# Optimization experiments

Measured on AMD Instinct MI355X. Metric: run time of the kernel, lower is better.

Reference implementation:

```python
import jax, jax.numpy as jnp
import numpy as np

V, H, L = 32000, 2048, 4
B, S = 4, 1024


def setup_inputs() -> dict:
    key = jax.random.key(0)
    ks = jax.random.split(key, 10)
    input_ids = jax.random.randint(ks[0], (B, S), 0, V)
    emb = jax.random.normal(ks[1], (V, H), dtype=jnp.float32)
    # ternary quantized weights in {-1, 0, +1}, stored as int8
    layer_wq = jax.random.randint(ks[2], (L, H, H), -1, 2).astype(jnp.int8)
    layer_scale = jax.random.normal(ks[3], (L, H, 1), dtype=jnp.float32)
    layer_bias = jax.random.normal(ks[4], (L, H), dtype=jnp.float32)
    out_wq = jax.random.randint(ks[5], (V, H), -1, 2).astype(jnp.int8)
    out_scale = jax.random.normal(ks[6], (V, 1), dtype=jnp.float32)
    out_bias = jax.random.normal(ks[7], (V,), dtype=jnp.float32)
    return {
        "input_ids": input_ids,
        "emb": emb,
        "layer_wq": layer_wq,
        "layer_scale": layer_scale,
        "layer_bias": layer_bias,
        "out_wq": out_wq,
        "out_scale": out_scale,
        "out_bias": out_bias,
    }


def _bit_linear(x, wq, scale, bias):
    # dequantize ternary int8 weight: [out,in] * [out,1] -> fp32, then x @ W^T + b
    w = wq.astype(jnp.float32) * scale
    return jnp.einsum("bsh,oh->bso", x, w) + bias


def reference(input_ids, emb, layer_wq, layer_scale, layer_bias, out_wq, out_scale, out_bias):
    x = emb[input_ids]  # [B,S,H]
    for i in range(L):
        x = jax.nn.relu(_bit_linear(x, layer_wq[i], layer_scale[i], layer_bias[i]))
    logits = _bit_linear(x, out_wq, out_scale, out_bias)  # [B,S,V]
    return logits
```

## Files before the change

kernel.cpp:

```cpp
#include <hip/hip_runtime.h>
#include <hip/hip_bf16.h>
#include <stdint.h>
#include <stddef.h>

#define GLOBAL_AS __attribute__((address_space(1)))
#define LDS_AS __attribute__((address_space(3)))

typedef __attribute__((ext_vector_type(4))) float f32x4;
typedef __attribute__((ext_vector_type(8))) short bf16x8;
typedef __attribute__((ext_vector_type(4))) int   i32x4;

template<int N> struct ICn { static constexpr int value = N; };

__device__ __forceinline__ unsigned short f2bf(float f) {
  unsigned u = __float_as_uint(f);
  u += 0x7FFFu + ((u >> 16) & 1u);
  return (unsigned short)(u >> 16);
}

__device__ __forceinline__ void load_lds16(const void* g, void* l) {
  __builtin_amdgcn_global_load_lds((const GLOBAL_AS void*)g, (LDS_AS void*)l, 16, 0, 0);
}

template<int IMM, typename T>
__device__ __forceinline__ void ds_read128t(T &d, unsigned addr) {
  asm volatile("ds_read_b128 %0, %1 offset:%c2"
               : "=&v"(d) : "v"(addr), "i"(IMM));
}

#define SBAR0 __builtin_amdgcn_sched_barrier(0)

#define WAITV(N) do { SBAR0; \
  asm volatile("s_waitcnt vmcnt(" #N ")" ::: "memory"); SBAR0; } while (0)

#define WAITVL(N) do { SBAR0; \
  asm volatile("s_waitcnt vmcnt(" #N ") lgkmcnt(0)" ::: "memory"); SBAR0; } while (0)

#define LGKMW(N) do { SBAR0; \
  asm volatile("s_waitcnt lgkmcnt(" #N ")" ::: "memory"); SBAR0; } while (0)

__global__ __launch_bounds__(256) void detect_dtype_k(const int* __restrict__ w,
                                                      int* __restrict__ flag) {
  __shared__ int bad;
  if (threadIdx.x == 0) bad = 0;
  __syncthreads();
  int b = 0;
  for (int i = threadIdx.x; i < 4096; i += 256) {
    int v = w[i];
    if (v < -1 || v > 1) b = 1;
  }
  if (b) bad = 1;
  __syncthreads();
  if (threadIdx.x == 0) *flag = bad ? 0 : 1;
}

__global__ __launch_bounds__(256) void gather_emb_k(const int* __restrict__ ids,
                                                    const float* __restrict__ emb,
                                                    unsigned short* __restrict__ x) {
  const int t = blockIdx.x;
  const int row = ids[t];
  const float4* src = (const float4*)(emb + (size_t)row * 2048);
  const int e = threadIdx.x;
  float4 a = src[e * 2], b = src[e * 2 + 1];
  uint4 o;
  o.x = f2bf(a.x) | ((unsigned)f2bf(a.y) << 16);
  o.y = f2bf(a.z) | ((unsigned)f2bf(a.w) << 16);
  o.z = f2bf(b.x) | ((unsigned)f2bf(b.y) << 16);
  o.w = f2bf(b.z) | ((unsigned)f2bf(b.w) << 16);
  *(uint4*)(x + (size_t)t * 2048 + e * 8) = o;
}

__global__ __launch_bounds__(256) void convert_w_k(const void* __restrict__ src,
                                                   unsigned short* __restrict__ dst,
                                                   const int* __restrict__ flag) {
  const long long idx = ((long long)blockIdx.x * 256 + threadIdx.x) * 8;
  int v[8];
  if (*flag) {
    const int* s = (const int*)src + idx;
    const int4 a = *(const int4*)s;
    const int4 b = *(const int4*)(s + 4);
    v[0] = a.x; v[1] = a.y; v[2] = a.z; v[3] = a.w;
    v[4] = b.x; v[5] = b.y; v[6] = b.z; v[7] = b.w;
  } else {
    const uint2 u = *(const uint2*)((const char*)src + idx);
    v[0] = (char)(u.x); v[1] = (char)(u.x >> 8); v[2] = (char)(u.x >> 16); v[3] = (char)(u.x >> 24);
    v[4] = (char)(u.y); v[5] = (char)(u.y >> 8); v[6] = (char)(u.y >> 16); v[7] = (char)(u.y >> 24);
  }
  unsigned short o[8];
  #pragma unroll
  for (int k = 0; k < 8; ++k)
    o[k] = (v[k] == 0) ? 0 : ((v[k] > 0) ? 0x3F80 : 0xBF80);
  uint4 w;
  w.x = o[0] | ((unsigned)o[1] << 16);
  w.y = o[2] | ((unsigned)o[3] << 16);
  w.z = o[4] | ((unsigned)o[5] << 16);
  w.w = o[6] | ((unsigned)o[7] << 16);
  *(uint4*)(dst + idx) = w;
}

__global__ __launch_bounds__(256) void pack_w8_k(const void* __restrict__ src,
                                                 signed char* __restrict__ dst,
                                                 const int* __restrict__ flag) {
  if (!*flag) return;
  const long long idx = ((long long)blockIdx.x * 256 + threadIdx.x) * 8;
  const int* s = (const int*)src + idx;
  const int4 a = *(const int4*)s;
  const int4 b = *(const int4*)(s + 4);
  uint2 o;
  o.x = ((unsigned)(unsigned char)(signed char)a.x)       |
        ((unsigned)(unsigned char)(signed char)a.y << 8)  |
        ((unsigned)(unsigned char)(signed char)a.z << 16) |
        ((unsigned)(unsigned char)(signed char)a.w << 24);
  o.y = ((unsigned)(unsigned char)(signed char)b.x)       |
        ((unsigned)(unsigned char)(signed char)b.y << 8)  |
        ((unsigned)(unsigned char)(signed char)b.z << 16) |
        ((unsigned)(unsigned char)(signed char)b.w << 24);
  *(uint2*)(dst + idx) = o;
}

__global__ __launch_bounds__(256) void colsum_k(const signed char* __restrict__ wp,
                                                const signed char* __restrict__ wr,
                                                const int* __restrict__ flag,
                                                float* __restrict__ cs) {
  const signed char* w = (*flag) ? wp : wr;
  const int lane = threadIdx.x & 63;
  const int c = blockIdx.x * 4 + (threadIdx.x >> 6);
  const int4* p = (const int4*)(w + (size_t)c * 2048 + lane * 32);
  const int4 a = p[0], b = p[1];
  int wds[8] = {a.x, a.y, a.z, a.w, b.x, b.y, b.z, b.w};
  int s = 0;
  #pragma unroll
  for (int k = 0; k < 8; ++k)
    #pragma unroll
    for (int bb = 0; bb < 4; ++bb)
      s += (signed char)(wds[k] >> (8 * bb));
  #pragma unroll
  for (int o = 32; o; o >>= 1) s += __shfl_xor(s, o);
  if (lane == 0) cs[c] = (float)s;
}

__global__ __launch_bounds__(256) void rowquant_k(const unsigned short* __restrict__ x,
                                                  signed char* __restrict__ xq,
                                                  float* __restrict__ srow) {
  __shared__ float wmax[4];
  const int r = blockIdx.x;
  const int e = threadIdx.x;
  const uint4 u = *(const uint4*)(x + (size_t)r * 2048 + e * 8);
  unsigned wds[4] = {u.x, u.y, u.z, u.w};
  float v[8];
  #pragma unroll
  for (int k = 0; k < 4; ++k) {
    v[2 * k]     = __uint_as_float(wds[k] << 16);
    v[2 * k + 1] = __uint_as_float(wds[k] & 0xFFFF0000u);
  }
  float m = 0.0f;
  #pragma unroll
  for (int k = 0; k < 8; ++k) m = fmaxf(m, v[k]);
  #pragma unroll
  for (int o = 32; o; o >>= 1) m = fmaxf(m, __shfl_xor(m, o));
  if ((threadIdx.x & 63) == 0) wmax[threadIdx.x >> 6] = m;
  __syncthreads();
  const float mx = fmaxf(fmaxf(wmax[0], wmax[1]), fmaxf(wmax[2], wmax[3]));
  const float inv = mx > 0.0f ? 255.0f / mx : 0.0f;
  unsigned b[8];
  #pragma unroll
  for (int k = 0; k < 8; ++k) {
    int q = __float2int_rn(v[k] * inv - 127.5f);
    q = q < -128 ? -128 : (q > 127 ? 127 : q);
    b[k] = (unsigned)(unsigned char)(signed char)q;
  }
  uint2 o;
  o.x = b[0] | (b[1] << 8) | (b[2] << 16) | (b[3] << 24);
  o.y = b[4] | (b[5] << 8) | (b[6] << 16) | (b[7] << 24);
  *(uint2*)(xq + (size_t)r * 2048 + e * 8) = o;
  if (threadIdx.x == 0) srow[r] = mx * (1.0f / 255.0f);
}

__global__ __launch_bounds__(256, 2) void gemm_bt2_k(
    const unsigned short* __restrict__ A,
    const unsigned short* __restrict__ Bw,
    const float* __restrict__ scale,
    const float* __restrict__ bias,
    unsigned short* __restrict__ Cout,
    int M, int N, int K)
{
  __shared__ unsigned short As[2 * 8192];
  __shared__ unsigned short Bs[2 * 8192];

  const int tid  = threadIdx.x;
  const int lane = tid & 63;
  const int wid  = tid >> 6;
  const int wm   = wid >> 1;
  const int wn   = wid & 1;
  const int l15  = lane & 15;
  const int l4   = lane >> 4;

  const int mBase = blockIdx.y * 128;
  const int nBase = blockIdx.x * 128;

  const int gsw = ((lane & 7) ^ (lane >> 3)) * 8;

  const unsigned asB = (unsigned)(size_t)(const LDS_AS unsigned short*)As;
  const unsigned bsB = (unsigned)(size_t)(const LDS_AS unsigned short*)Bs;
  const unsigned x7  = (unsigned)(l15 & 7);
  const unsigned vA0 = asB + (wm << 13) + l15 * 128 + ((((unsigned)l4    ) ^ x7) << 4);
  const unsigned vA1 = asB + (wm << 13) + l15 * 128 + ((((unsigned)l4 + 4) ^ x7) << 4);
  const unsigned vB0 = bsB + (wn << 13) + l15 * 128 + ((((unsigned)l4    ) ^ x7) << 4);
  const unsigned vB1 = bsB + (wn << 13) + l15 * 128 + ((((unsigned)l4 + 4) ^ x7) << 4);

  const unsigned short* pA[4];
  const unsigned short* pB[4];
  #pragma unroll
  for (int j = 0; j < 4; ++j) {
    const int row = (wid * 4 + j) * 8 + (lane >> 3);
    pA[j] = A  + (size_t)(mBase + row) * K + gsw;
    pB[j] = Bw + (size_t)(nBase + row) * K + gsw;
  }

  f32x4 acc[4][4];
  #pragma unroll
  for (int i = 0; i < 4; ++i)
    #pragma unroll
    for (int j = 0; j < 4; ++j)
      acc[i][j] = (f32x4){0.f, 0.f, 0.f, 0.f};

  const int nt = K >> 6;

  #pragma unroll
  for (int j = 0; j < 4; ++j)
    load_lds16(pA[j], As + (wid * 4 + j) * 512);
  #pragma unroll
  for (int j = 0; j < 4; ++j)
    load_lds16(pB[j], Bs + (wid * 4 + j) * 512);
  #pragma unroll
  for (int j = 0; j < 4; ++j) { pA[j] += 64; pB[j] += 64; }
  WAITV(0);
  __builtin_amdgcn_s_barrier();

  bf16x8 afA[4], afB[4], bfrA[4], bfrB[4];

  for (int t = 0; t < nt; ++t) {
    const unsigned po = (unsigned)(t & 1) * 16384u;
    const unsigned aA0 = vA0 + po, aA1 = vA1 + po;
    const unsigned aB0 = vB0 + po, aB1 = vB1 + po;
    unsigned short* dA = As + (size_t)((t + 1) & 1) * 8192;
    unsigned short* dB = Bs + (size_t)((t + 1) & 1) * 8192;
    const bool st = (t + 1 < nt);

    ds_read128t<0   >(afA[0], aA0); ds_read128t<2048>(afA[1], aA0);
    ds_read128t<4096>(afA[2], aA0); ds_read128t<6144>(afA[3], aA0);
    ds_read128t<0   >(bfrA[0], aB0); ds_read128t<2048>(bfrA[1], aB0);
    ds_read128t<4096>(bfrA[2], aB0); ds_read128t<6144>(bfrA[3], aB0);
    ds_read128t<0   >(afB[0], aA1); ds_read128t<2048>(afB[1], aA1);
    ds_read128t<4096>(afB[2], aA1); ds_read128t<6144>(afB[3], aA1);
    ds_read128t<0   >(bfrB[0], aB1); ds_read128t<2048>(bfrB[1], aB1);
    ds_read128t<4096>(bfrB[2], aB1); ds_read128t<6144>(bfrB[3], aB1);
    #pragma unroll
    for (int j = 0; j < 4; ++j)
      load_lds16(st ? pA[j] : A, dA + (wid * 4 + j) * 512);
    #pragma unroll
    for (int j = 0; j < 4; ++j)
      load_lds16(st ? pB[j] : Bw, dB + (wid * 4 + j) * 512);
    #pragma unroll
    for (int j = 0; j < 4; ++j) { pA[j] += 64; pB[j] += 64; }

    LGKMW(8);
    __builtin_amdgcn_s_setprio(1);
    #pragma unroll
    for (int i = 0; i < 4; ++i)
      #pragma unroll
      for (int j = 0; j < 4; ++j)
        acc[i][j] = __builtin_amdgcn_mfma_f32_16x16x32_bf16(afA[i], bfrA[j], acc[i][j], 0, 0, 0);
    __builtin_amdgcn_s_setprio(0);
    SBAR0;
    LGKMW(0);
    __builtin_amdgcn_s_setprio(1);
    #pragma unroll
    for (int i = 0; i < 4; ++i)
      #pragma unroll
      for (int j = 0; j < 4; ++j)
        acc[i][j] = __builtin_amdgcn_mfma_f32_16x16x32_bf16(afB[i], bfrB[j], acc[i][j], 0, 0, 0);
    __builtin_amdgcn_s_setprio(0);
    SBAR0;
    WAITV(0);
    __builtin_amdgcn_s_barrier();
  }

  const int lr = l4;
  const int lc = l15;
  #pragma unroll
  for (int j = 0; j < 4; ++j) {
    const int col = nBase + wn * 64 + j * 16 + lc;
    const float sc = scale[col];
    const float bs = bias[col];
    #pragma unroll
    for (int i = 0; i < 4; ++i) {
      const int r0 = mBase + wm * 64 + i * 16 + lr * 4;
      #pragma unroll
      for (int r = 0; r < 4; ++r) {
        float vv = fmaxf(acc[i][j][r] * sc + bs, 0.0f);
        Cout[(size_t)(r0 + r) * N + col] = f2bf(vv);
      }
    }
  }
}


#define RD_B8() do { \
  ds_read128t<PAR*32768 +    0>(bfr[0][0], vB0); ds_read128t<PAR*32768 +    0>(bfr[0][1], vB1); \
  ds_read128t<PAR*32768 + 2048>(bfr[1][0], vB0); ds_read128t<PAR*32768 + 2048>(bfr[1][1], vB1); \
  ds_read128t<PAR*32768 + 4096>(bfr[2][0], vB0); ds_read128t<PAR*32768 + 4096>(bfr[2][1], vB1); \
  ds_read128t<PAR*32768 + 6144>(bfr[3][0], vB0); ds_read128t<PAR*32768 + 6144>(bfr[3][1], vB1); \
} while (0)

#define RD_A2(dst, R) do { \
  ds_read128t<PAR*32768 + (R)*2048       >(dst[0][0], vA0); ds_read128t<PAR*32768 + (R)*2048       >(dst[0][1], vA1); \
  ds_read128t<PAR*32768 + (R)*2048 + 2048>(dst[1][0], vA0); ds_read128t<PAR*32768 + (R)*2048 + 2048>(dst[1][1], vA1); \
} while (0)

#define STAGE_A(h) do { if (t >= 1 && t + 1 < nt) { \
  load_lds16(pA[h][0], Asf + (PAR ^ 1) * 32768 + (h) * 16384 +        wid * 1024); \
  load_lds16(pA[h][1], Asf + (PAR ^ 1) * 32768 + (h) * 16384 + 8192 + wid * 1024); \
  pA[h][0] += 128; pA[h][1] += 128; } } while (0)

#define STAGE_B(h) do { if (t + 2 < nt) { \
  load_lds16(pB[h][0], Bsf + PAR * 32768 + (h) * 16384 +        wid * 1024); \
  load_lds16(pB[h][1], Bsf + PAR * 32768 + (h) * 16384 + 8192 + wid * 1024); \
  pB[h][0] += 128; pB[h][1] += 128; } } while (0)

#define MFMA_PH(IP, AF) do { \
  __builtin_amdgcn_s_setprio(1); \
  { _Pragma("unroll") for (int ii = 0; ii < 2; ++ii) { \
      _Pragma("unroll") for (int j = 0; j < 4; ++j) { \
        acc[(IP)*2+ii][j] = __builtin_amdgcn_mfma_i32_16x16x64_i8(AF[ii][0], bfr[j][0], acc[(IP)*2+ii][j], 0, 0, 0); \
        acc[(IP)*2+ii][j] = __builtin_amdgcn_mfma_i32_16x16x64_i8(AF[ii][1], bfr[j][1], acc[(IP)*2+ii][j], 0, 0, 0); \
  } } } \
  __builtin_amdgcn_s_setprio(0); \
  SBAR0; \
} while (0)

__global__ __launch_bounds__(512, 2) void gemm256i8_k(
    const signed char* __restrict__ Aq,
    const signed char* __restrict__ Bpk,
    const signed char* __restrict__ Braw,
    const int* __restrict__ flag,
    const float* __restrict__ scale,
    const float* __restrict__ bias,
    const float* __restrict__ srow,
    const float* __restrict__ colsum,
    float* __restrict__ C,
    int M, int N, int K)
{
  __shared__ signed char Asf[2 * 32768];
  __shared__ signed char Bsf[2 * 32768];

  const signed char* Bq = (*flag) ? Bpk : Braw;

  const int tid  = threadIdx.x;
  const int lane = tid & 63;
  const int wid  = tid >> 6;
  const int wm   = wid >> 2;
  const int wn   = wid & 3;
  const int l15  = lane & 15;
  const int l4   = lane >> 4;

  const int q    = gridDim.x >> 3;
  const int wgid = (blockIdx.x & 7) * q + (blockIdx.x >> 3);
  const int mBase = (wgid & 15) << 8;
  const int nBase = (wgid >> 4) << 8;

  const int gsw = ((lane & 7) ^ (lane >> 3)) * 16;

  const unsigned asB = (unsigned)(size_t)(const LDS_AS signed char*)Asf;
  const unsigned bsB = (unsigned)(size_t)(const LDS_AS signed char*)Bsf;
  const unsigned x7  = (unsigned)(l15 & 7);
  const unsigned vA0 = asB + (wm << 14) + l15 * 128 + ((((unsigned)l4    ) ^ x7) << 4);
  const unsigned vA1 = asB + (wm << 14) + l15 * 128 + ((((unsigned)l4 + 4) ^ x7) << 4);
  const unsigned vB0 = bsB + (wn << 13) + l15 * 128 + ((((unsigned)l4    ) ^ x7) << 4);
  const unsigned vB1 = bsB + (wn << 13) + l15 * 128 + ((((unsigned)l4 + 4) ^ x7) << 4);

  const signed char* pA[2][2];
  const signed char* pB[2][2];
  #pragma unroll
  for (int h = 0; h < 2; ++h)
    #pragma unroll
    for (int j = 0; j < 2; ++j) {
      const int row = h * 128 + j * 64 + wid * 8 + (lane >> 3);
      pA[h][j] = Aq + (size_t)(mBase + row) * K + gsw;
      pB[h][j] = Bq + (size_t)(nBase + row) * K + gsw;
    }

  i32x4 acc[8][4];
  #pragma unroll
  for (int i = 0; i < 8; ++i)
    #pragma unroll
    for (int j = 0; j < 4; ++j)
      acc[i][j] = (i32x4){0, 0, 0, 0};

  const int nt = K >> 7;

  #pragma unroll
  for (int h = 0; h < 2; ++h)
    #pragma unroll
    for (int j = 0; j < 2; ++j)
      load_lds16(pA[h][j], Asf + h * 16384 + j * 8192 + wid * 1024);
  #pragma unroll
  for (int h = 0; h < 2; ++h)
    #pragma unroll
    for (int j = 0; j < 2; ++j)
      load_lds16(pB[h][j], Bsf + h * 16384 + j * 8192 + wid * 1024);
  #pragma unroll
  for (int h = 0; h < 2; ++h)
    #pragma unroll
    for (int j = 0; j < 2; ++j)
      load_lds16(pA[h][j] + 128, Asf + 32768 + h * 16384 + j * 8192 + wid * 1024);
  #pragma unroll
  for (int h = 0; h < 2; ++h)
    #pragma unroll
    for (int j = 0; j < 2; ++j)
      load_lds16(pB[h][j] + 128, Bsf + 32768 + h * 16384 + j * 8192 + wid * 1024);
  #pragma unroll
  for (int h = 0; h < 2; ++h)
    #pragma unroll
    for (int j = 0; j < 2; ++j) { pA[h][j] += 256; pB[h][j] += 256; }

  asm volatile("s_waitcnt vmcnt(8)" ::: "memory");
  __builtin_amdgcn_s_barrier();

  i32x4 bfr[4][2];
  i32x4 afP[2][2], afQ[2][2];

  auto tile_body = [&](int t, auto par_c) {
    constexpr int PAR = decltype(par_c)::value;
    RD_A2(afP, 0);
    RD_B8();
    RD_A2(afQ, 2);
    STAGE_A(0);
    LGKMW(4);
    MFMA_PH(0, afP);
    RD_A2(afP, 4);
    STAGE_A(1);
    LGKMW(4);
    MFMA_PH(1, afQ);
    __builtin_amdgcn_s_barrier();
    RD_A2(afQ, 6);
    STAGE_B(0);
    LGKMW(4);
    MFMA_PH(2, afP);
    STAGE_B(1);
    LGKMW(0);
    MFMA_PH(3, afQ);
    if (t + 2 < nt) { WAITV(4); }
    else            { WAITV(0); }
    __builtin_amdgcn_s_barrier();
  };

  for (int t = 0; t < nt; t += 2) {
    tile_body(t,     ICn<0>{});
    tile_body(t + 1, ICn<1>{});
  }

  #pragma unroll
  for (int j = 0; j < 4; ++j) {
    const int col = nBase + wn * 64 + j * 16 + l15;
    const float sc  = scale[col];
    const float csc = colsum[col] * sc;
    const float bs  = bias[col];
    #pragma unroll
    for (int i = 0; i < 8; ++i) {
      const int r0 = mBase + wm * 128 + i * 16 + l4 * 4;
      const f32x4 sv = *(const f32x4*)(srow + r0);
      #pragma unroll
      for (int r = 0; r < 4; ++r) {
        const float fa = (float)acc[i][j][r];
        C[(size_t)(r0 + r) * N + col] =
            fmaf(fa, sv[r] * sc, fmaf(127.5f * sv[r], csc, bs));
      }
    }
  }
}

extern "C" void kernel_launch(void* const* d_in, const int* in_sizes, int n_in,
                              void* d_out, int out_size, void* d_ws, size_t ws_size,
                              hipStream_t stream) {
  const int V = 32000, H = 2048, L = 4, M = 4096;
  const int*   ids         = (const int*)d_in[0];
  const float* emb         = (const float*)d_in[1];
  const void*  layer_wq    = d_in[2];
  const float* layer_scale = (const float*)d_in[3];
  const float* layer_bias  = (const float*)d_in[4];
  const void*  out_wq      = d_in[5];
  const float* out_scale   = (const float*)d_in[6];
  const float* out_bias    = (const float*)d_in[7];
  float* out = (float*)d_out;

  char* ws = (char*)d_ws;
  const size_t xBytes = (size_t)M * H * 2;
  unsigned short* xA  = (unsigned short*)(ws);
  unsigned short* xB  = (unsigned short*)(ws + xBytes);
  unsigned short* lw  = (unsigned short*)(ws + 2 * xBytes);
  size_t off = 2 * xBytes + (size_t)L * H * H * 2;
  signed char* ow8    = (signed char*)(ws + off);   off += (size_t)V * H;
  signed char* xq     = (signed char*)(ws + off);   off += (size_t)M * H;
  float* srow         = (float*)(ws + off);         off += (size_t)M * 4;
  float* cs           = (float*)(ws + off);         off += (size_t)V * 4;
  int* flag           = (int*)(ws + off);

  detect_dtype_k<<<1, 256, 0, stream>>>((const int*)layer_wq, flag);
  gather_emb_k<<<M, 256, 0, stream>>>(ids, emb, xA);
  convert_w_k<<<(L * H * H) / 2048, 256, 0, stream>>>(layer_wq, lw, flag);
  pack_w8_k<<<(V * H) / 2048, 256, 0, stream>>>(out_wq, ow8, flag);
  colsum_k<<<V / 4, 256, 0, stream>>>(ow8, (const signed char*)out_wq, flag, cs);

  dim3 blk(256);
  dim3 gh(H / 128, M / 128);
  unsigned short* xin = xA;
  unsigned short* xout = xB;
  for (int i = 0; i < L; ++i) {
    gemm_bt2_k<<<gh, blk, 0, stream>>>(xin, lw + (size_t)i * H * H,
                                       layer_scale + i * H, layer_bias + i * H,
                                       xout, M, H, H);
    unsigned short* t = xin; xin = xout; xout = t;
  }

  rowquant_k<<<M, 256, 0, stream>>>(xin, xq, srow);

  gemm256i8_k<<<dim3(2000), dim3(512), 0, stream>>>(
      xq, ow8, (const signed char*)out_wq, flag,
      out_scale, out_bias, srow, cs, out, M, V, H);
}
```

Before: 631.1 us.

## Use 16-wave workgroups with smaller per-wave tiles in output int8 GEMM

Restructures the final int8 logits GEMM to launch 1024 threads (16 waves) per 256x256 tile, so each wave owns a 64x64 sub-tile instead of 128x64. Accumulator registers are halved, and the A/B staging is simplified to one pointer per operand with a single-stage prefetch that waits for all loads each tile. The inner schedule now reads all A fragments up front and streams B column fragments. This trades deeper prefetch and register reuse for more waves per CU to hide latency. It risks lower arithmetic intensity per wave and more barrier cost from the full vmcnt wait every tile.

Result: slower. 1.185 ms (+87.8%).

```diff
diff --git a/kernel.cpp b/kernel.cpp
--- a/kernel.cpp
+++ b/kernel.cpp
@@ -306,40 +306,37 @@
 }
 
 
-#define RD_B8() do { \
-  ds_read128t<PAR*32768 +    0>(bfr[0][0], vB0); ds_read128t<PAR*32768 +    0>(bfr[0][1], vB1); \
-  ds_read128t<PAR*32768 + 2048>(bfr[1][0], vB0); ds_read128t<PAR*32768 + 2048>(bfr[1][1], vB1); \
-  ds_read128t<PAR*32768 + 4096>(bfr[2][0], vB0); ds_read128t<PAR*32768 + 4096>(bfr[2][1], vB1); \
-  ds_read128t<PAR*32768 + 6144>(bfr[3][0], vB0); ds_read128t<PAR*32768 + 6144>(bfr[3][1], vB1); \
+#define RD_AF8() do { \
+  ds_read128t<PAR*32768 +    0>(af[0][0], vA0); ds_read128t<PAR*32768 +    0>(af[0][1], vA1); \
+  ds_read128t<PAR*32768 + 2048>(af[1][0], vA0); ds_read128t<PAR*32768 + 2048>(af[1][1], vA1); \
+  ds_read128t<PAR*32768 + 4096>(af[2][0], vA0); ds_read128t<PAR*32768 + 4096>(af[2][1], vA1); \
+  ds_read128t<PAR*32768 + 6144>(af[3][0], vA0); ds_read128t<PAR*32768 + 6144>(af[3][1], vA1); \
 } while (0)
 
-#define RD_A2(dst, R) do { \
-  ds_read128t<PAR*32768 + (R)*2048       >(dst[0][0], vA0); ds_read128t<PAR*32768 + (R)*2048       >(dst[0][1], vA1); \
-  ds_read128t<PAR*32768 + (R)*2048 + 2048>(dst[1][0], vA0); ds_read128t<PAR*32768 + (R)*2048 + 2048>(dst[1][1], vA1); \
+#define RD_BCOL(DST, J) do { \
+  ds_read128t<PAR*32768 + (J)*2048>(DST[0], vB0); \
+  ds_read128t<PAR*32768 + (J)*2048>(DST[1], vB1); \
 } while (0)
 
-#define STAGE_A(h) do { if (t >= 1 && t + 1 < nt) { \
-  load_lds16(pA[h][0], Asf + (PAR ^ 1) * 32768 + (h) * 16384 +        wid * 1024); \
-  load_lds16(pA[h][1], Asf + (PAR ^ 1) * 32768 + (h) * 16384 + 8192 + wid * 1024); \
-  pA[h][0] += 128; pA[h][1] += 128; } } while (0)
-
-#define STAGE_B(h) do { if (t + 2 < nt) { \
-  load_lds16(pB[h][0], Bsf + PAR * 32768 + (h) * 16384 +        wid * 1024); \
-  load_lds16(pB[h][1], Bsf + PAR * 32768 + (h) * 16384 + 8192 + wid * 1024); \
-  pB[h][0] += 128; pB[h][1] += 128; } } while (0)
-
-#define MFMA_PH(IP, AF) do { \
+#define MFMA_COL(J, B) do { \
   __builtin_amdgcn_s_setprio(1); \
-  { _Pragma("unroll") for (int ii = 0; ii < 2; ++ii) { \
-      _Pragma("unroll") for (int j = 0; j < 4; ++j) { \
-        acc[(IP)*2+ii][j] = __builtin_amdgcn_mfma_i32_16x16x64_i8(AF[ii][0], bfr[j][0], acc[(IP)*2+ii][j], 0, 0, 0); \
-        acc[(IP)*2+ii][j] = __builtin_amdgcn_mfma_i32_16x16x64_i8(AF[ii][1], bfr[j][1], acc[(IP)*2+ii][j], 0, 0, 0); \
-  } } } \
+  { _Pragma("unroll") for (int i_ = 0; i_ < 4; ++i_) { \
+      acc[i_][J] = __builtin_amdgcn_mfma_i32_16x16x64_i8(af[i_][0], B[0], acc[i_][J], 0, 0, 0); \
+      acc[i_][J] = __builtin_amdgcn_mfma_i32_16x16x64_i8(af[i_][1], B[1], acc[i_][J], 0, 0, 0); \
+  } } \
   __builtin_amdgcn_s_setprio(0); \
   SBAR0; \
 } while (0)
 
-__global__ __launch_bounds__(512, 2) void gemm256i8_k(
+#define STAGE16(PARD) do { \
+  load_lds16(st ? pA           : Aq, Asf + (PARD) * 32768 + wid * 2048); \
+  load_lds16(st ? (pA + 16384) : Aq, Asf + (PARD) * 32768 + wid * 2048 + 1024); \
+  load_lds16(st ? pB           : Bq, Bsf + (PARD) * 32768 + wid * 2048); \
+  load_lds16(st ? (pB + 16384) : Bq, Bsf + (PARD) * 32768 + wid * 2048 + 1024); \
+  pA += 128; pB += 128; \
+} while (0)
+
+__global__ __launch_bounds__(1024, 4) void gemm256i8_k(
     const signed char* __restrict__ Aq,
     const signed char* __restrict__ Bpk,
     const signed char* __restrict__ Braw,
@@ -374,84 +371,55 @@
   const unsigned asB = (unsigned)(size_t)(const LDS_AS signed char*)Asf;
   const unsigned bsB = (unsigned)(size_t)(const LDS_AS signed char*)Bsf;
   const unsigned x7  = (unsigned)(l15 & 7);
-  const unsigned vA0 = asB + (wm << 14) + l15 * 128 + ((((unsigned)l4    ) ^ x7) << 4);
-  const unsigned vA1 = asB + (wm << 14) + l15 * 128 + ((((unsigned)l4 + 4) ^ x7) << 4);
+  const unsigned vA0 = asB + (wm << 13) + l15 * 128 + ((((unsigned)l4    ) ^ x7) << 4);
+  const unsigned vA1 = asB + (wm << 13) + l15 * 128 + ((((unsigned)l4 + 4) ^ x7) << 4);
   const unsigned vB0 = bsB + (wn << 13) + l15 * 128 + ((((unsigned)l4    ) ^ x7) << 4);
   const unsigned vB1 = bsB + (wn << 13) + l15 * 128 + ((((unsigned)l4 + 4) ^ x7) << 4);
 
-  const signed char* pA[2][2];
-  const signed char* pB[2][2];
-  #pragma unroll
-  for (int h = 0; h < 2; ++h)
-    #pragma unroll
-    for (int j = 0; j < 2; ++j) {
-      const int row = h * 128 + j * 64 + wid * 8 + (lane >> 3);
-      pA[h][j] = Aq + (size_t)(mBase + row) * K + gsw;
-      pB[h][j] = Bq + (size_t)(nBase + row) * K + gsw;
-    }
-
-  i32x4 acc[8][4];
-  #pragma unroll
-  for (int i = 0; i < 8; ++i)
+  const signed char* pA = Aq + (size_t)(mBase + wid * 16 + (lane >> 3)) * K + gsw;
+  const signed char* pB = Bq + (size_t)(nBase + wid * 16 + (lane >> 3)) * K + gsw;
+
+  i32x4 acc[4][4];
+  #pragma unroll
+  for (int i = 0; i < 4; ++i)
     #pragma unroll
     for (int j = 0; j < 4; ++j)
       acc[i][j] = (i32x4){0, 0, 0, 0};
 
   const int nt = K >> 7;
 
-  #pragma unroll
-  for (int h = 0; h < 2; ++h)
-    #pragma unroll
-    for (int j = 0; j < 2; ++j)
-      load_lds16(pA[h][j], Asf + h * 16384 + j * 8192 + wid * 1024);
-  #pragma unroll
-  for (int h = 0; h < 2; ++h)
-    #pragma unroll
-    for (int j = 0; j < 2; ++j)
-      load_lds16(pB[h][j], Bsf + h * 16384 + j * 8192 + wid * 1024);
-  #pragma unroll
-  for (int h = 0; h < 2; ++h)
-    #pragma unroll
-    for (int j = 0; j < 2; ++j)
-      load_lds16(pA[h][j] + 128, Asf + 32768 + h * 16384 + j * 8192 + wid * 1024);
-  #pragma unroll
-  for (int h = 0; h < 2; ++h)
-    #pragma unroll
-    for (int j = 0; j < 2; ++j)
-      load_lds16(pB[h][j] + 128, Bsf + 32768 + h * 16384 + j * 8192 + wid * 1024);
-  #pragma unroll
-  for (int h = 0; h < 2; ++h)
-    #pragma unroll
-    for (int j = 0; j < 2; ++j) { pA[h][j] += 256; pB[h][j] += 256; }
-
-  asm volatile("s_waitcnt vmcnt(8)" ::: "memory");
+  i32x4 af[4][2], bP[2], bQ[2];
+
+  {
+    const bool st = true; (void)st;
+    load_lds16(pA,         Asf + wid * 2048);
+    load_lds16(pA + 16384, Asf + wid * 2048 + 1024);
+    load_lds16(pB,         Bsf + wid * 2048);
+    load_lds16(pB + 16384, Bsf + wid * 2048 + 1024);
+    pA += 128; pB += 128;
+  }
+  WAITV(0);
   __builtin_amdgcn_s_barrier();
-
-  i32x4 bfr[4][2];
-  i32x4 afP[2][2], afQ[2][2];
 
   auto tile_body = [&](int t, auto par_c) {
     constexpr int PAR = decltype(par_c)::value;
-    RD_A2(afP, 0);
-    RD_B8();
-    RD_A2(afQ, 2);
-    STAGE_A(0);
-    LGKMW(4);
-    MFMA_PH(0, afP);
-    RD_A2(afP, 4);
-    STAGE_A(1);
-    LGKMW(4);
-    MFMA_PH(1, afQ);
-    __builtin_amdgcn_s_barrier();
-    RD_A2(afQ, 6);
-    STAGE_B(0);
-    LGKMW(4);
-    MFMA_PH(2, afP);
-    STAGE_B(1);
+    const bool st = (t + 1 < nt);
+    RD_AF8();
+    RD_BCOL(bP, 0);
+    RD_BCOL(bQ, 1);
+    SBAR0;
+    STAGE16(PAR ^ 1);
+    LGKMW(2);
+    MFMA_COL(0, bP);
+    RD_BCOL(bP, 2);
+    LGKMW(2);
+    MFMA_COL(1, bQ);
+    RD_BCOL(bQ, 3);
+    LGKMW(2);
+    MFMA_COL(2, bP);
     LGKMW(0);
-    MFMA_PH(3, afQ);
-    if (t + 2 < nt) { WAITV(4); }
-    else            { WAITV(0); }
+    MFMA_COL(3, bQ);
+    WAITV(0);
     __builtin_amdgcn_s_barrier();
   };
 
@@ -459,6 +427,8 @@
     tile_body(t,     ICn<0>{});
     tile_body(t + 1, ICn<1>{});
   }
+
+  WAITVL(0);
 
   #pragma unroll
   for (int j = 0; j < 4; ++j) {
@@ -467,8 +437,8 @@
     const float csc = colsum[col] * sc;
     const float bs  = bias[col];
     #pragma unroll
-    for (int i = 0; i < 8; ++i) {
-      const int r0 = mBase + wm * 128 + i * 16 + l4 * 4;
+    for (int i = 0; i < 4; ++i) {
+      const int r0 = mBase + wm * 64 + i * 16 + l4 * 4;
       const f32x4 sv = *(const f32x4*)(srow + r0);
       #pragma unroll
       for (int r = 0; r < 4; ++r) {
@@ -525,7 +495,7 @@
 
   rowquant_k<<<M, 256, 0, stream>>>(xin, xq, srow);
 
-  gemm256i8_k<<<dim3(2000), dim3(512), 0, stream>>>(
+  gemm256i8_k<<<dim3(2000), dim3(1024), 0, stream>>>(
       xq, ow8, (const signed char*)out_wq, flag,
       out_scale, out_bias, srow, cs, out, M, V, H);
 }
```
